# Kernel tuning notes

Measured on AMD Instinct MI355X. Metric: run time of the kernel, lower is better.

The kernel has to match this reference:

```python
import jax, jax.numpy as jnp
import numpy as np

LN_EPS = 1e-5
KERNEL_EPS = 1e-6


def setup_inputs() -> dict:
    key = jax.random.key(0)
    kx, kw, kb = jax.random.split(key, 3)
    B, N, D, H = 8, 2048, 256, 4
    x = jax.random.normal(kx, (B, N, D), dtype=jnp.float32) * 0.05
    log_sigmas = jnp.zeros((H, 1, 1), dtype=jnp.float32)
    W = jax.random.normal(kw, (D, D), dtype=jnp.float32) * 0.05  # torch Linear weight (out, in)
    b = jax.random.normal(kb, (D,), dtype=jnp.float32) * 0.05
    gamma = jnp.ones((D,), dtype=jnp.float32)
    beta = jnp.zeros((D,), dtype=jnp.float32)
    return {"x": x, "log_sigmas": log_sigmas, "W": W, "b": b, "gamma": gamma, "beta": beta}


def _layer_norm(y, gamma, beta):
    mu = jnp.mean(y, axis=-1, keepdims=True)
    var = jnp.var(y, axis=-1, keepdims=True)
    return (y - mu) * jax.lax.rsqrt(var + LN_EPS) * gamma + beta


def reference(x, log_sigmas, W, b, gamma, beta):
    # pairwise squared euclidean distances: (B, N, N)
    sq = jnp.sum(x * x, axis=-1)
    dist_sq = sq[:, :, None] + sq[:, None, :] - 2.0 * jnp.einsum('bnd,bmd->bnm', x, x)
    dist_sq = jnp.maximum(dist_sq, 0.0)
    # per-head Gaussian kernel adjacency, mean over heads
    sigmas = jnp.exp(log_sigmas)                      # (H,1,1)
    denom = 2.0 * sigmas ** 2 + KERNEL_EPS            # (H,1,1)
    adjs = jnp.exp(-dist_sq[:, None] / denom[None])   # (B,H,N,N)
    adj_final = jnp.mean(adjs, axis=1)                # (B,N,N)
    # aggregate, project, activate, residual layernorm
    out = jnp.einsum('bnm,bmd->bnd', adj_final, x)
    out = out @ W.T + b
    res = _layer_norm(jax.nn.elu(out) + x, gamma, beta)
    return res
```

## Files before the change

### kernel.cpp

```cpp
#include <hip/hip_runtime.h>

typedef unsigned short u16;
typedef __attribute__((ext_vector_type(8))) short bf16x8;
typedef __attribute__((ext_vector_type(4))) float f32x4;
typedef __attribute__((ext_vector_type(8))) unsigned short u16x8;

#define DEVI static __device__ __forceinline__

constexpr int Bb = 8, Nn = 2048, Dd = 256;

DEVI u16 f2bf(float f) {
    unsigned int u = __builtin_bit_cast(unsigned int, f);
    u = (u + 0x7fffu + ((u >> 16) & 1u)) >> 16;
    return (u16)u;
}
DEVI float bf2f(u16 v) {
    return __builtin_bit_cast(float, (unsigned int)v << 16);
}

DEVI void gl_lds16(const void* g, void* l) {
    __builtin_amdgcn_global_load_lds(
        (const __attribute__((address_space(1))) unsigned int*)g,
        (__attribute__((address_space(3))) unsigned int*)l, 16, 0, 0);
}

__global__ void prep_x_kernel(const float* __restrict__ x, u16* __restrict__ xb,
                              float* __restrict__ sq) {
    int row = blockIdx.x * 4 + (threadIdx.x >> 6);
    int l = threadIdx.x & 63;
    const float4 v = *(const float4*)(x + (size_t)row * Dd + l * 4);
    float ss = v.x * v.x + v.y * v.y + v.z * v.z + v.w * v.w;
    ushort4 o;
    o.x = f2bf(v.x); o.y = f2bf(v.y); o.z = f2bf(v.z); o.w = f2bf(v.w);
    *(ushort4*)(xb + (size_t)row * Dd + l * 4) = o;
#pragma unroll
    for (int s = 1; s < 64; s <<= 1) ss += __shfl_xor(ss, s);
    if (l == 0) sq[row] = ss;
}

__global__ void prep_w_kernel(const float* __restrict__ W, u16* __restrict__ Wb) {
    int i = (blockIdx.x * 256 + threadIdx.x) * 4;
    const float4 v = *(const float4*)(W + i);
    ushort4 o;
    o.x = f2bf(v.x); o.y = f2bf(v.y); o.z = f2bf(v.z); o.w = f2bf(v.w);
    *(ushort4*)(Wb + i) = o;
}

__global__ void prep_t_kernel(const u16* __restrict__ xb, u16* __restrict__ xbt) {
    int nt = blockIdx.x, dt = blockIdx.y, b = blockIdx.z;
    int n0 = nt * 64, d0 = dt * 64;
    __shared__ __align__(16) u16 tile[64 * 64];
    int t = threadIdx.x;
#pragma unroll
    for (int p = 0; p < 2; ++p) {
        int row = p * 32 + (t >> 3);
        int c8 = t & 7;
        uint4 v = *(const uint4*)(xb + ((size_t)(b * Nn + n0 + row)) * Dd + d0 + c8 * 8);
        *(uint4*)((char*)tile + row * 128 + ((c8 * 16) ^ ((row & 7) << 4))) = v;
    }
    __syncthreads();
#pragma unroll
    for (int p = 0; p < 2; ++p) {
        int d = p * 32 + (t >> 3);
        int nn = (t & 7) * 8;
        u16x8 vv;
#pragma unroll
        for (int e = 0; e < 8; ++e) {
            int row = nn + e;
            vv[e] = *(const u16*)((char*)tile + row * 128 + ((d * 2) ^ ((row & 7) << 4)));
        }
        *(u16x8*)(xbt + ((size_t)(b * Dd + d0 + d)) * Nn + n0 + nn) = vv;
    }
}

__global__ __launch_bounds__(512, 1) void fused_adj_kernel(
    const u16* __restrict__ xb, const u16* __restrict__ xbt,
    const float* __restrict__ sq, const float* __restrict__ lsig,
    u16* __restrict__ opart) {
    int bid = blockIdx.x;
    int xcd = bid & 7, j = bid >> 3;
    int g = xcd + 8 * (j >> 3);
    int nt8 = j & 7;
    int b = g >> 2, q = g & 3;
    int r0 = b * Nn + nt8 * 256;
    int m0b = b * Nn + q * 512;

    int tid = threadIdx.x;
    int w = tid >> 6, l = tid & 63;
    int l15 = l & 15, lhi = l >> 4;

    __shared__ __align__(16) char smem[98304];
    char* sXm = smem;
    char* sXmt = smem + 32768;
    char* sP = smem + 65536 + w * 4096;

    float nc[4];
#pragma unroll
    for (int h = 0; h < 4; ++h) {
        float denom = 2.f * expf(2.f * lsig[h]) + 1e-6f;
        nc[h] = -1.44269504f / denom;
    }
    bool uniform = (lsig[0] == lsig[1]) && (lsig[1] == lsig[2]) && (lsig[2] == lsig[3]);

    bf16x8 bf[2][8];
    float sqn[2];
#pragma unroll
    for (int rg = 0; rg < 2; ++rg) {
        const u16* xr = xb + (size_t)(r0 + w * 32 + rg * 16 + l15) * Dd;
#pragma unroll
        for (int kt = 0; kt < 8; ++kt) bf[rg][kt] = *(const bf16x8*)(xr + kt * 32 + lhi * 8);
        sqn[rg] = sq[r0 + w * 32 + rg * 16 + l15];
    }

    f32x4 of[2][16];
#pragma unroll
    for (int rg = 0; rg < 2; ++rg)
#pragma unroll
        for (int dt = 0; dt < 16; ++dt) of[rg][dt] = (f32x4){0.f, 0.f, 0.f, 0.f};

    int swz = (l15 & 7) << 4;

    for (int t = 0; t < 8; ++t) {
        int m0 = m0b + t * 64;
        __syncthreads();
#pragma unroll
        for (int it = 0; it < 4; ++it) {
            int c0 = it * 512 + w * 64;
            int c = c0 + l;
            int row = c >> 5, c16 = c & 31;
            gl_lds16(xb + (size_t)(m0 + row) * Dd + (c16 ^ (row & 7)) * 8, sXm + c0 * 16);
        }
#pragma unroll
        for (int it = 0; it < 4; ++it) {
            int c0 = it * 512 + w * 64;
            int c = c0 + l;
            int row = c >> 3, c16 = c & 7;
            gl_lds16(xbt + (size_t)(b * Dd + row) * Nn + (q * 512 + t * 64) + (c16 ^ (row & 7)) * 8,
                     sXmt + c0 * 16);
        }
        __syncthreads();

#pragma unroll
        for (int mt = 0; mt < 4; ++mt) {
            float4 sqm = *(const float4*)(sq + m0 + mt * 16 + lhi * 4);
            f32x4 sfv[2];
            sfv[0] = (f32x4){0.f, 0.f, 0.f, 0.f};
            sfv[1] = (f32x4){0.f, 0.f, 0.f, 0.f};
#pragma unroll
            for (int kt = 0; kt < 8; ++kt) {
                bf16x8 av = *(const bf16x8*)(sXm + (mt * 16 + l15) * 512 +
                                             ((kt * 64 + lhi * 16) ^ swz));
                sfv[0] = __builtin_amdgcn_mfma_f32_16x16x32_bf16(av, bf[0][kt], sfv[0], 0, 0, 0);
                sfv[1] = __builtin_amdgcn_mfma_f32_16x16x32_bf16(av, bf[1][kt], sfv[1], 0, 0, 0);
            }
            float sm[4] = {sqm.x, sqm.y, sqm.z, sqm.w};
#pragma unroll
            for (int rg = 0; rg < 2; ++rg) {
                ushort4 pk;
#pragma unroll
                for (int r = 0; r < 4; ++r) {
                    float d2 = fmaxf(fmaf(-2.f, sfv[rg][r], sqn[rg] + sm[r]), 0.f);
                    float p = exp2f(d2 * nc[0]);
                    if (!uniform)
                        p = 0.25f * (p + exp2f(d2 * nc[1]) + exp2f(d2 * nc[2]) + exp2f(d2 * nc[3]));
                    ((u16*)&pk)[r] = f2bf(p);
                }
                int n = rg * 16 + l15;
                *(ushort4*)(sP + n * 128 + ((mt * 32 + lhi * 8) ^ ((n & 7) << 4))) = pk;
            }
        }

#pragma unroll
        for (int kt2 = 0; kt2 < 2; ++kt2) {
            bf16x8 pa0 = *(const bf16x8*)(sP + l15 * 128 + ((kt2 * 64 + lhi * 16) ^ swz));
            bf16x8 pa1 = *(const bf16x8*)(sP + (16 + l15) * 128 + ((kt2 * 64 + lhi * 16) ^ swz));
#pragma unroll
            for (int dt = 0; dt < 16; ++dt) {
                bf16x8 bv = *(const bf16x8*)(sXmt + (dt * 16 + l15) * 128 +
                                             ((kt2 * 64 + lhi * 16) ^ swz));
                of[0][dt] = __builtin_amdgcn_mfma_f32_16x16x32_bf16(pa0, bv, of[0][dt], 0, 0, 0);
                of[1][dt] = __builtin_amdgcn_mfma_f32_16x16x32_bf16(pa1, bv, of[1][dt], 0, 0, 0);
            }
        }
    }

    u16* od = opart + (size_t)q * ((size_t)Bb * Nn * Dd);
#pragma unroll
    for (int rg = 0; rg < 2; ++rg)
#pragma unroll
        for (int dt = 0; dt < 16; ++dt)
#pragma unroll
            for (int r = 0; r < 4; ++r) {
                size_t row = (size_t)(r0 + w * 32 + rg * 16 + lhi * 4 + r);
                od[row * Dd + dt * 16 + l15] = f2bf(of[rg][dt][r]);
            }
}

__global__ __launch_bounds__(512, 1) void proj_ln_kernel(
    const u16* __restrict__ opart, const u16* __restrict__ Wb,
    const float* __restrict__ x, const float* __restrict__ bvec,
    const float* __restrict__ gamma, const float* __restrict__ beta,
    float* __restrict__ out) {
    int tid = threadIdx.x, w = tid >> 6, l = tid & 63;
    int rg = w & 3, h = w >> 2;
    int lrow = l & 15, lhi = l >> 4;
    size_t row0 = (size_t)blockIdx.x * 64 + rg * 16;
    const size_t QS = (size_t)Bb * Nn * Dd;

    __shared__ __align__(16) float xch[8 * 16 * 2 * 64];

    f32x4 acc[16];
#pragma unroll
    for (int jt = 0; jt < 16; ++jt) acc[jt] = (f32x4){0.f, 0.f, 0.f, 0.f};

#pragma unroll
    for (int kk = 0; kk < 4; ++kk) {
        int kc = h * 4 + kk;
        float as[8] = {0.f, 0.f, 0.f, 0.f, 0.f, 0.f, 0.f, 0.f};
#pragma unroll
        for (int qq = 0; qq < 4; ++qq) {
            u16x8 v = *(const u16x8*)(opart + QS * qq + (row0 + lrow) * Dd + kc * 32 + lhi * 8);
#pragma unroll
            for (int e = 0; e < 8; ++e) as[e] += bf2f(v[e]);
        }
        bf16x8 a;
#pragma unroll
        for (int e = 0; e < 8; ++e) a[e] = (short)f2bf(as[e]);
#pragma unroll
        for (int jt = 0; jt < 16; ++jt) {
            bf16x8 bv = *(const bf16x8*)(Wb + (size_t)(jt * 16 + lrow) * Dd + kc * 32 + lhi * 8);
            acc[jt] = __builtin_amdgcn_mfma_f32_16x16x32_bf16(a, bv, acc[jt], 0, 0, 0);
        }
    }

#pragma unroll
    for (int jt = 0; jt < 16; ++jt)
#pragma unroll
        for (int qq = 0; qq < 2; ++qq) {
            int r = (1 - h) * 2 + qq;
            xch[(w * 16 + jt) * 128 + qq * 64 + l] = acc[jt][r];
        }
    __syncthreads();
#pragma unroll
    for (int jt = 0; jt < 16; ++jt)
#pragma unroll
        for (int qq = 0; qq < 2; ++qq)
            acc[jt][h * 2 + qq] += xch[((w ^ 4) * 16 + jt) * 128 + qq * 64 + l];

#pragma unroll
    for (int qq = 0; qq < 2; ++qq) {
        int r = h * 2 + qq;
        size_t grow = row0 + lhi * 4 + r;
        float vbuf[16];
        float s1 = 0.f, s2 = 0.f;
#pragma unroll
        for (int jt = 0; jt < 16; ++jt) {
            int jcol = jt * 16 + lrow;
            float v = acc[jt][r] + bvec[jcol];
            float e = v > 0.f ? v : (exp2f(v * 1.44269504f) - 1.f);
            float res = e + x[grow * Dd + jcol];
            vbuf[jt] = res;
            s1 += res;
            s2 += res * res;
        }
#pragma unroll
        for (int m = 1; m < 16; m <<= 1) {
            s1 += __shfl_xor(s1, m);
            s2 += __shfl_xor(s2, m);
        }
        float mean = s1 * (1.f / 256.f);
        float var = s2 * (1.f / 256.f) - mean * mean;
        float rstd = rsqrtf(var + 1e-5f);
#pragma unroll
        for (int jt = 0; jt < 16; ++jt) {
            int jcol = jt * 16 + lrow;
            out[grow * Dd + jcol] = (vbuf[jt] - mean) * rstd * gamma[jcol] + beta[jcol];
        }
    }
}

extern "C" void kernel_launch(void* const* d_in, const int* in_sizes, int n_in,
                              void* d_out, int out_size, void* d_ws, size_t ws_size,
                              hipStream_t stream) {
    const float* x = (const float*)d_in[0];
    const float* lsig = (const float*)d_in[1];
    const float* W = (const float*)d_in[2];
    const float* bvec = (const float*)d_in[3];
    const float* gamma = (const float*)d_in[4];
    const float* beta = (const float*)d_in[5];
    float* out = (float*)d_out;

    char* ws = (char*)d_ws;
    u16* xb = (u16*)ws;
    u16* xbt = (u16*)(ws + 8388608);
    float* sq = (float*)(ws + 16777216);
    u16* Wb = (u16*)(ws + 16842752);
    u16* opart = (u16*)(ws + 16973824);

    prep_x_kernel<<<dim3(Bb * Nn / 4), dim3(256), 0, stream>>>(x, xb, sq);
    prep_w_kernel<<<dim3(64), dim3(256), 0, stream>>>(W, Wb);
    prep_t_kernel<<<dim3(Nn / 64, Dd / 64, Bb), dim3(256), 0, stream>>>(xb, xbt);
    fused_adj_kernel<<<dim3(256), dim3(512), 0, stream>>>(xb, xbt, sq, lsig, opart);
    proj_ln_kernel<<<dim3(Bb * Nn / 64), dim3(512), 0, stream>>>(opart, Wb, x, bvec, gamma, beta, out);
}
```

Baseline: 95.37 us.

## Double-buffer LDS tiles in adjacency kernel and fuse x prep with transpose

The fused adjacency kernel now double-buffers its xb and xbt tiles in LDS. The next tile is loaded asynchronously with partial vmcnt waits while the current tile is computed, replacing the load-then-sync-then-compute loop. The x conversion, squared-norm and transpose prep kernels are merged into one, which saves a launch and a re-read of xb. The block-to-batch mapping is changed, and the residual in the projection kernel now reads bf16 x instead of fp32, which cuts traffic but lowers residual precision. The larger LDS footprint (160KB) and the hand-counted vmcnt values are risks.

```diff
diff --git a/kernel.cpp b/kernel.cpp
--- a/kernel.cpp
+++ b/kernel.cpp
@@ -24,18 +24,44 @@
         (__attribute__((address_space(3))) unsigned int*)l, 16, 0, 0);
 }
 
-__global__ void prep_x_kernel(const float* __restrict__ x, u16* __restrict__ xb,
-                              float* __restrict__ sq) {
-    int row = blockIdx.x * 4 + (threadIdx.x >> 6);
-    int l = threadIdx.x & 63;
-    const float4 v = *(const float4*)(x + (size_t)row * Dd + l * 4);
-    float ss = v.x * v.x + v.y * v.y + v.z * v.z + v.w * v.w;
-    ushort4 o;
-    o.x = f2bf(v.x); o.y = f2bf(v.y); o.z = f2bf(v.z); o.w = f2bf(v.w);
-    *(ushort4*)(xb + (size_t)row * Dd + l * 4) = o;
-#pragma unroll
-    for (int s = 1; s < 64; s <<= 1) ss += __shfl_xor(ss, s);
-    if (l == 0) sq[row] = ss;
+__global__ __launch_bounds__(256) void prep_xt_kernel(
+    const float* __restrict__ x, u16* __restrict__ xb, u16* __restrict__ xbt,
+    float* __restrict__ sq) {
+    int n0 = blockIdx.x * 64;
+    int b = blockIdx.y;
+    int t = threadIdx.x;
+    __shared__ __align__(16) u16 tile[64 * 256];
+    int row = t >> 2;
+    int c0 = (t & 3) * 64;
+    const float* xr = x + ((size_t)(b * Nn + n0 + row)) * Dd + c0;
+    u16* xbr = xb + ((size_t)(b * Nn + n0 + row)) * Dd + c0;
+    float ss = 0.f;
+#pragma unroll
+    for (int cc = 0; cc < 16; ++cc) {
+        float4 v = *(const float4*)(xr + cc * 4);
+        ss += v.x * v.x + v.y * v.y + v.z * v.z + v.w * v.w;
+        ushort4 o;
+        o.x = f2bf(v.x); o.y = f2bf(v.y); o.z = f2bf(v.z); o.w = f2bf(v.w);
+        *(ushort4*)(xbr + cc * 4) = o;
+        int cb = (c0 + cc * 4) * 2;
+        *(ushort4*)((char*)tile + row * 512 + (cb ^ ((row & 7) << 4))) = o;
+    }
+    ss += __shfl_xor(ss, 1);
+    ss += __shfl_xor(ss, 2);
+    if ((t & 3) == 0) sq[b * Nn + n0 + row] = ss;
+    __syncthreads();
+#pragma unroll
+    for (int p = 0; p < 8; ++p) {
+        int d = p * 32 + (t >> 3);
+        int n8 = (t & 7) * 8;
+        u16x8 vv;
+#pragma unroll
+        for (int e = 0; e < 8; ++e) {
+            int r2 = n8 + e;
+            vv[e] = *(const u16*)((char*)tile + r2 * 512 + ((d * 2) ^ ((r2 & 7) << 4)));
+        }
+        *(u16x8*)(xbt + ((size_t)(b * Dd + d)) * Nn + n0 + n8) = vv;
+    }
 }
 
 __global__ void prep_w_kernel(const float* __restrict__ W, u16* __restrict__ Wb) {
@@ -46,53 +72,29 @@
     *(ushort4*)(Wb + i) = o;
 }
 
-__global__ void prep_t_kernel(const u16* __restrict__ xb, u16* __restrict__ xbt) {
-    int nt = blockIdx.x, dt = blockIdx.y, b = blockIdx.z;
-    int n0 = nt * 64, d0 = dt * 64;
-    __shared__ __align__(16) u16 tile[64 * 64];
-    int t = threadIdx.x;
-#pragma unroll
-    for (int p = 0; p < 2; ++p) {
-        int row = p * 32 + (t >> 3);
-        int c8 = t & 7;
-        uint4 v = *(const uint4*)(xb + ((size_t)(b * Nn + n0 + row)) * Dd + d0 + c8 * 8);
-        *(uint4*)((char*)tile + row * 128 + ((c8 * 16) ^ ((row & 7) << 4))) = v;
-    }
-    __syncthreads();
-#pragma unroll
-    for (int p = 0; p < 2; ++p) {
-        int d = p * 32 + (t >> 3);
-        int nn = (t & 7) * 8;
-        u16x8 vv;
-#pragma unroll
-        for (int e = 0; e < 8; ++e) {
-            int row = nn + e;
-            vv[e] = *(const u16*)((char*)tile + row * 128 + ((d * 2) ^ ((row & 7) << 4)));
-        }
-        *(u16x8*)(xbt + ((size_t)(b * Dd + d0 + d)) * Nn + n0 + nn) = vv;
-    }
-}
-
 __global__ __launch_bounds__(512, 1) void fused_adj_kernel(
     const u16* __restrict__ xb, const u16* __restrict__ xbt,
     const float* __restrict__ sq, const float* __restrict__ lsig,
     u16* __restrict__ opart) {
     int bid = blockIdx.x;
-    int xcd = bid & 7, j = bid >> 3;
-    int g = xcd + 8 * (j >> 3);
-    int nt8 = j & 7;
-    int b = g >> 2, q = g & 3;
+    int b = bid & 7;
+    int j = bid >> 3;
+    int q = j & 3;
+    int nt8 = j >> 2;
     int r0 = b * Nn + nt8 * 256;
     int m0b = b * Nn + q * 512;
+    int mq0 = q * 512;
 
     int tid = threadIdx.x;
     int w = tid >> 6, l = tid & 63;
     int l15 = l & 15, lhi = l >> 4;
 
-    __shared__ __align__(16) char smem[98304];
-    char* sXm = smem;
-    char* sXmt = smem + 32768;
-    char* sP = smem + 65536 + w * 4096;
+    __shared__ __align__(16) char smem[163840];
+    char* sXmA = smem;
+    char* sXmB = smem + 32768;
+    char* sXmtA = smem + 65536;
+    char* sXmtB = smem + 98304;
+    char* sP = smem + 131072 + w * 4096;
 
     float nc[4];
 #pragma unroll
@@ -120,69 +122,93 @@
 
     int swz = (l15 & 7) << 4;
 
-    for (int t = 0; t < 8; ++t) {
-        int m0 = m0b + t * 64;
-        __syncthreads();
-#pragma unroll
-        for (int it = 0; it < 4; ++it) {
-            int c0 = it * 512 + w * 64;
-            int c = c0 + l;
-            int row = c >> 5, c16 = c & 31;
-            gl_lds16(xb + (size_t)(m0 + row) * Dd + (c16 ^ (row & 7)) * 8, sXm + c0 * 16);
-        }
-#pragma unroll
-        for (int it = 0; it < 4; ++it) {
-            int c0 = it * 512 + w * 64;
-            int c = c0 + l;
-            int row = c >> 3, c16 = c & 7;
-            gl_lds16(xbt + (size_t)(b * Dd + row) * Nn + (q * 512 + t * 64) + (c16 ^ (row & 7)) * 8,
-                     sXmt + c0 * 16);
-        }
-        __syncthreads();
-
-#pragma unroll
-        for (int mt = 0; mt < 4; ++mt) {
-            float4 sqm = *(const float4*)(sq + m0 + mt * 16 + lhi * 4);
-            f32x4 sfv[2];
-            sfv[0] = (f32x4){0.f, 0.f, 0.f, 0.f};
-            sfv[1] = (f32x4){0.f, 0.f, 0.f, 0.f};
-#pragma unroll
-            for (int kt = 0; kt < 8; ++kt) {
-                bf16x8 av = *(const bf16x8*)(sXm + (mt * 16 + l15) * 512 +
-                                             ((kt * 64 + lhi * 16) ^ swz));
-                sfv[0] = __builtin_amdgcn_mfma_f32_16x16x32_bf16(av, bf[0][kt], sfv[0], 0, 0, 0);
-                sfv[1] = __builtin_amdgcn_mfma_f32_16x16x32_bf16(av, bf[1][kt], sfv[1], 0, 0, 0);
-            }
-            float sm[4] = {sqm.x, sqm.y, sqm.z, sqm.w};
-#pragma unroll
-            for (int rg = 0; rg < 2; ++rg) {
-                ushort4 pk;
-#pragma unroll
-                for (int r = 0; r < 4; ++r) {
-                    float d2 = fmaxf(fmaf(-2.f, sfv[rg][r], sqn[rg] + sm[r]), 0.f);
-                    float p = exp2f(d2 * nc[0]);
-                    if (!uniform)
-                        p = 0.25f * (p + exp2f(d2 * nc[1]) + exp2f(d2 * nc[2]) + exp2f(d2 * nc[3]));
-                    ((u16*)&pk)[r] = f2bf(p);
-                }
-                int n = rg * 16 + l15;
-                *(ushort4*)(sP + n * 128 + ((mt * 32 + lhi * 8) ^ ((n & 7) << 4))) = pk;
-            }
-        }
-
-#pragma unroll
-        for (int kt2 = 0; kt2 < 2; ++kt2) {
-            bf16x8 pa0 = *(const bf16x8*)(sP + l15 * 128 + ((kt2 * 64 + lhi * 16) ^ swz));
-            bf16x8 pa1 = *(const bf16x8*)(sP + (16 + l15) * 128 + ((kt2 * 64 + lhi * 16) ^ swz));
-#pragma unroll
-            for (int dt = 0; dt < 16; ++dt) {
-                bf16x8 bv = *(const bf16x8*)(sXmt + (dt * 16 + l15) * 128 +
-                                             ((kt2 * 64 + lhi * 16) ^ swz));
-                of[0][dt] = __builtin_amdgcn_mfma_f32_16x16x32_bf16(pa0, bv, of[0][dt], 0, 0, 0);
-                of[1][dt] = __builtin_amdgcn_mfma_f32_16x16x32_bf16(pa1, bv, of[1][dt], 0, 0, 0);
-            }
-        }
-    }
+#define STAGE(SXM, SXMT, tt) {                                                \
+    int m0_ = m0b + (tt) * 64;                                                \
+    int mc0_ = mq0 + (tt) * 64;                                               \
+    _Pragma("unroll") for (int it = 0; it < 4; ++it) {                        \
+        int c0 = it * 512 + w * 64;                                           \
+        int c = c0 + l;                                                       \
+        int row = c >> 5, c16 = c & 31;                                       \
+        gl_lds16(xb + (size_t)(m0_ + row) * Dd + (c16 ^ (row & 7)) * 8,       \
+                 (SXM) + c0 * 16);                                            \
+    }                                                                          \
+    _Pragma("unroll") for (int it = 0; it < 4; ++it) {                        \
+        int c0 = it * 512 + w * 64;                                           \
+        int c = c0 + l;                                                       \
+        int row = c >> 3, c16 = c & 7;                                        \
+        gl_lds16(xbt + (size_t)(b * Dd + row) * Nn + mc0_ + (c16 ^ (row & 7)) * 8, \
+                 (SXMT) + c0 * 16);                                           \
+    } }
+
+#define LOADSQ(SQV, tt) {                                                     \
+    _Pragma("unroll") for (int mt = 0; mt < 4; ++mt)                          \
+        SQV[mt] = *(const float4*)(sq + m0b + (tt) * 64 + mt * 16 + lhi * 4); \
+    }
+
+#define COMPUTE(SXM, SXMT, SQV) {                                             \
+    _Pragma("unroll") for (int mt = 0; mt < 4; ++mt) {                        \
+        f32x4 sfv0 = (f32x4){0.f, 0.f, 0.f, 0.f};                             \
+        f32x4 sfv1 = (f32x4){0.f, 0.f, 0.f, 0.f};                             \
+        _Pragma("unroll") for (int kt = 0; kt < 8; ++kt) {                    \
+            bf16x8 av = *(const bf16x8*)((SXM) + (mt * 16 + l15) * 512 +      \
+                                         ((kt * 64 + lhi * 16) ^ swz));       \
+            sfv0 = __builtin_amdgcn_mfma_f32_16x16x32_bf16(av, bf[0][kt], sfv0, 0, 0, 0); \
+            sfv1 = __builtin_amdgcn_mfma_f32_16x16x32_bf16(av, bf[1][kt], sfv1, 0, 0, 0); \
+        }                                                                      \
+        float sm[4] = {SQV[mt].x, SQV[mt].y, SQV[mt].z, SQV[mt].w};           \
+        _Pragma("unroll") for (int rg = 0; rg < 2; ++rg) {                    \
+            f32x4 sfv = rg ? sfv1 : sfv0;                                     \
+            ushort4 pk;                                                       \
+            _Pragma("unroll") for (int r = 0; r < 4; ++r) {                   \
+                float d2 = fmaxf(fmaf(-2.f, sfv[r], sqn[rg] + sm[r]), 0.f);   \
+                float p = exp2f(d2 * nc[0]);                                  \
+                if (!uniform)                                                 \
+                    p = 0.25f * (p + exp2f(d2 * nc[1]) + exp2f(d2 * nc[2]) + exp2f(d2 * nc[3])); \
+                ((u16*)&pk)[r] = f2bf(p);                                     \
+            }                                                                  \
+            int n_ = rg * 16 + l15;                                           \
+            *(ushort4*)(sP + n_ * 128 + ((mt * 32 + lhi * 8) ^ ((n_ & 7) << 4))) = pk; \
+        }                                                                      \
+    }                                                                          \
+    _Pragma("unroll") for (int kt2 = 0; kt2 < 2; ++kt2) {                     \
+        bf16x8 pa0 = *(const bf16x8*)(sP + l15 * 128 + ((kt2 * 64 + lhi * 16) ^ swz)); \
+        bf16x8 pa1 = *(const bf16x8*)(sP + (16 + l15) * 128 + ((kt2 * 64 + lhi * 16) ^ swz)); \
+        _Pragma("unroll") for (int dt = 0; dt < 16; ++dt) {                   \
+            bf16x8 bv = *(const bf16x8*)((SXMT) + (dt * 16 + l15) * 128 +     \
+                                         ((kt2 * 64 + lhi * 16) ^ swz));      \
+            of[0][dt] = __builtin_amdgcn_mfma_f32_16x16x32_bf16(pa0, bv, of[0][dt], 0, 0, 0); \
+            of[1][dt] = __builtin_amdgcn_mfma_f32_16x16x32_bf16(pa1, bv, of[1][dt], 0, 0, 0); \
+        }                                                                      \
+    } }
+
+    float4 sqvA[4], sqvB[4];
+
+    STAGE(sXmA, sXmtA, 0)
+    LOADSQ(sqvA, 0)
+
+    for (int tt = 0; tt < 4; ++tt) {
+        int t0 = tt * 2;
+        STAGE(sXmB, sXmtB, t0 + 1)
+        LOADSQ(sqvB, t0 + 1)
+        asm volatile("s_waitcnt vmcnt(12)" ::: "memory");
+        __builtin_amdgcn_s_barrier();
+        COMPUTE(sXmA, sXmtA, sqvA)
+        __builtin_amdgcn_s_barrier();
+        if (tt < 3) {
+            STAGE(sXmA, sXmtA, t0 + 2)
+            LOADSQ(sqvA, t0 + 2)
+            asm volatile("s_waitcnt vmcnt(12)" ::: "memory");
+        } else {
+            asm volatile("s_waitcnt vmcnt(0)" ::: "memory");
+        }
+        __builtin_amdgcn_s_barrier();
+        COMPUTE(sXmB, sXmtB, sqvB)
+        __builtin_amdgcn_s_barrier();
+    }
+
+#undef STAGE
+#undef LOADSQ
+#undef COMPUTE
 
     u16* od = opart + (size_t)q * ((size_t)Bb * Nn * Dd);
 #pragma unroll
@@ -198,7 +224,7 @@
 
 __global__ __launch_bounds__(512, 1) void proj_ln_kernel(
     const u16* __restrict__ opart, const u16* __restrict__ Wb,
-    const float* __restrict__ x, const float* __restrict__ bvec,
+    const u16* __restrict__ xbres, const float* __restrict__ bvec,
     const float* __restrict__ gamma, const float* __restrict__ beta,
     float* __restrict__ out) {
     int tid = threadIdx.x, w = tid >> 6, l = tid & 63;
@@ -258,7 +284,7 @@
             int jcol = jt * 16 + lrow;
             float v = acc[jt][r] + bvec[jcol];
             float e = v > 0.f ? v : (exp2f(v * 1.44269504f) - 1.f);
-            float res = e + x[grow * Dd + jcol];
+            float res = e + bf2f(xbres[grow * Dd + jcol]);
             vbuf[jt] = res;
             s1 += res;
             s2 += res * res;
@@ -297,9 +323,8 @@
     u16* Wb = (u16*)(ws + 16842752);
     u16* opart = (u16*)(ws + 16973824);
 
-    prep_x_kernel<<<dim3(Bb * Nn / 4), dim3(256), 0, stream>>>(x, xb, sq);
+    prep_xt_kernel<<<dim3(Nn / 64, Bb), dim3(256), 0, stream>>>(x, xb, xbt, sq);
     prep_w_kernel<<<dim3(64), dim3(256), 0, stream>>>(W, Wb);
-    prep_t_kernel<<<dim3(Nn / 64, Dd / 64, Bb), dim3(256), 0, stream>>>(xb, xbt);
     fused_adj_kernel<<<dim3(256), dim3(512), 0, stream>>>(xb, xbt, sq, lsig, opart);
-    proj_ln_kernel<<<dim3(Bb * Nn / 64), dim3(512), 0, stream>>>(opart, Wb, x, bvec, gamma, beta, out);
-}
+    proj_ln_kernel<<<dim3(Bb * Nn / 64), dim3(512), 0, stream>>>(opart, Wb, xb, bvec, gamma, beta, out);
+}
```

After: 180.6 us. +89.3%, slower.
